# Optimization experiments

Measured on AMD Instinct MI355X. Metric: run time of the kernel, lower is better.

## Reference

```python
import jax, jax.numpy as jnp
import numpy as np

B, T, C = 16, 4096, 1024
MAX_POS, PAD_IDX = 8192, 1


def setup_inputs() -> dict:
    key = jax.random.key(0)
    ks = jax.random.split(key, 6)
    x = jax.random.normal(ks[0], (B, T, C), dtype=jnp.float32)
    lengths = jax.random.randint(ks[1], (B,), 1, T, dtype=jnp.int32)
    padding_mask = jnp.arange(T, dtype=jnp.int32)[None, :] >= lengths[:, None]
    bos_emb = jax.random.normal(ks[2], (C,), dtype=jnp.float32) * 0.02
    eos_emb = jax.random.normal(ks[3], (C,), dtype=jnp.float32) * 0.02
    pos_table = jax.random.normal(ks[4], (MAX_POS + PAD_IDX + 1, C), dtype=jnp.float32) * 0.02
    pos_table = pos_table.at[PAD_IDX].set(0.0)  # padding_idx row is zero in nn.Embedding
    ln_weight = jnp.ones((C,), dtype=jnp.float32)
    ln_bias = jnp.zeros((C,), dtype=jnp.float32)
    return {"x": x, "padding_mask": padding_mask, "lengths": lengths,
            "bos_emb": bos_emb, "eos_emb": eos_emb, "pos_table": pos_table,
            "ln_weight": ln_weight, "ln_bias": ln_bias}


def reference(x, padding_mask, lengths, bos_emb, eos_emb, pos_table, ln_weight, ln_bias):
    b, t, c = x.shape
    # prepend BOS, append a zero slot  -> (B, T+2, C)
    x = jnp.concatenate([
        jnp.broadcast_to(bos_emb, (b, 1, c)).astype(x.dtype),
        x,
        jnp.zeros((b, 1, c), dtype=x.dtype),
    ], axis=1)
    # vectorized per-row EOS scatter: x[i, lengths[i]+1, :] = eos_emb
    x = x.at[jnp.arange(b), lengths + 1].set(eos_emb.astype(x.dtype))
    new_lengths = lengths + 2
    pad_mask = jnp.arange(t + 2, dtype=jnp.int32)[None, :] >= new_lengths[:, None]  # (B, T+2)
    # fairseq make_positions on padding_mask.long() with padding_idx=1:
    # mask = input.ne(padding_idx) -> non-pad; positions = cumsum(mask)*mask + padding_idx
    nonpad = (~pad_mask).astype(jnp.int32)
    positions = jnp.cumsum(nonpad, axis=1) * nonpad + PAD_IDX  # pad slots -> index 1 (zero row)
    pos = pos_table[positions]  # (B, T+2, C)
    y = x + pos
    # LayerNorm over C, eps=1e-5
    mu = jnp.mean(y, axis=-1, keepdims=True)
    var = jnp.mean(jnp.square(y - mu), axis=-1, keepdims=True)
    y = (y - mu) * jax.lax.rsqrt(var + 1e-5) * ln_weight + ln_bias
    return y, pad_mask, new_lengths
```

## Files before the change

kernel.cpp:

```cpp
#include <hip/hip_runtime.h>
#include <hip/hip_bf16.h>

#define B_ 16
#define T_ 4096
#define C_ 1024
#define TP2 (T_ + 2)
#define NROWS (B_ * TP2)

typedef float float4v __attribute__((ext_vector_type(4)));

__global__ __launch_bounds__(256) void embed_ln_kernel(
    const float* __restrict__ x,
    const int*   __restrict__ lengths,
    const float* __restrict__ bos,
    const float* __restrict__ eos,
    const float* __restrict__ pos_table,
    const float* __restrict__ ln_w,
    const float* __restrict__ ln_b,
    float* __restrict__ out_y,
    float* __restrict__ out_mask,
    float* __restrict__ out_len)
{
    const int row  = blockIdx.x * 4 + (threadIdx.x >> 6);
    const int lane = threadIdx.x & 63;
    const int b    = row / TP2;
    const int t    = row - b * TP2;
    const int L    = lengths[b];

    float4v v[4];
    const float4v* srcv = nullptr;
    if (t == 0)          srcv = reinterpret_cast<const float4v*>(bos);
    else if (t == L + 1) srcv = reinterpret_cast<const float4v*>(eos);
    else if (t <= T_)    srcv = reinterpret_cast<const float4v*>(
                                    x + (size_t)(b * T_ + (t - 1)) * C_);
    if (srcv) {
        #pragma unroll
        for (int i = 0; i < 4; ++i)
            v[i] = __builtin_nontemporal_load(&srcv[i * 64 + lane]);
    } else {
        #pragma unroll
        for (int i = 0; i < 4; ++i)
            v[i] = (float4v)(0.f);
    }

    if (t <= L + 1) {
        const float4v* pr = reinterpret_cast<const float4v*>(
                                pos_table + (size_t)(t + 2) * C_);
        #pragma unroll
        for (int i = 0; i < 4; ++i)
            v[i] += pr[i * 64 + lane];
    }

    float s = 0.f, ss = 0.f;
    #pragma unroll
    for (int i = 0; i < 4; ++i) {
        s  += v[i].x + v[i].y + v[i].z + v[i].w;
        ss += v[i].x * v[i].x + v[i].y * v[i].y
            + v[i].z * v[i].z + v[i].w * v[i].w;
    }
    #pragma unroll
    for (int off = 32; off > 0; off >>= 1) {
        s  += __shfl_xor(s,  off);
        ss += __shfl_xor(ss, off);
    }
    const float inv_c = 1.0f / (float)C_;
    const float mu    = s * inv_c;
    const float var   = ss * inv_c - mu * mu;
    const float rstd  = rsqrtf(var + 1e-5f);

    float4v* dst = reinterpret_cast<float4v*>(out_y + (size_t)row * C_);
    const float4v* wv = reinterpret_cast<const float4v*>(ln_w);
    const float4v* bv = reinterpret_cast<const float4v*>(ln_b);
    #pragma unroll
    for (int i = 0; i < 4; ++i) {
        const float4v w  = wv[i * 64 + lane];
        const float4v bb = bv[i * 64 + lane];
        float4v o = (v[i] - mu) * rstd * w + bb;
        __builtin_nontemporal_store(o, &dst[i * 64 + lane]);
    }

    if (lane == 0) {
        out_mask[row] = (t >= L + 2) ? 1.0f : 0.0f;
        if (t == 0) out_len[b] = (float)(L + 2);
    }
}

extern "C" void kernel_launch(void* const* d_in, const int* in_sizes, int n_in,
                              void* d_out, int out_size, void* d_ws, size_t ws_size,
                              hipStream_t stream) {
    const float* x         = (const float*)d_in[0];
    const int*   lengths   = (const int*)d_in[2];
    const float* bos       = (const float*)d_in[3];
    const float* eos       = (const float*)d_in[4];
    const float* pos_table = (const float*)d_in[5];
    const float* ln_w      = (const float*)d_in[6];
    const float* ln_b      = (const float*)d_in[7];

    float* out_y    = (float*)d_out;
    float* out_mask = out_y + (size_t)B_ * TP2 * C_;
    float* out_len  = out_mask + (size_t)B_ * TP2;

    const int grid = NROWS / 4;
    embed_ln_kernel<<<grid, 256, 0, stream>>>(
        x, lengths, bos, eos, pos_table, ln_w, ln_b,
        out_y, out_mask, out_len);
}
```

Before: 102.8 us.

## Process four batches per wave sharing position row and LN params with double-buffered loads

```diff
diff --git a/kernel.cpp b/kernel.cpp
--- a/kernel.cpp
+++ b/kernel.cpp
@@ -5,7 +5,10 @@
 #define T_ 4096
 #define C_ 1024
 #define TP2 (T_ + 2)
-#define NROWS (B_ * TP2)
+#define BPW 4
+#define NGRP (B_ / BPW)
+#define NWAVES (TP2 * NGRP)
+#define NBLK (NWAVES / 4)
 
 typedef float float4v __attribute__((ext_vector_type(4)));
 
@@ -21,68 +24,92 @@
     float* __restrict__ out_mask,
     float* __restrict__ out_len)
 {
-    const int row  = blockIdx.x * 4 + (threadIdx.x >> 6);
+    const int wid  = blockIdx.x * 4 + (threadIdx.x >> 6);
     const int lane = threadIdx.x & 63;
-    const int b    = row / TP2;
-    const int t    = row - b * TP2;
-    const int L    = lengths[b];
+    const int t    = wid >> 2;
+    const int b0   = (wid & 3) * BPW;
 
-    float4v v[4];
-    const float4v* srcv = nullptr;
-    if (t == 0)          srcv = reinterpret_cast<const float4v*>(bos);
-    else if (t == L + 1) srcv = reinterpret_cast<const float4v*>(eos);
-    else if (t <= T_)    srcv = reinterpret_cast<const float4v*>(
-                                    x + (size_t)(b * T_ + (t - 1)) * C_);
-    if (srcv) {
+    float4v w[4], bb[4], ps[4];
+    {
+        const float4v* wv = reinterpret_cast<const float4v*>(ln_w);
+        const float4v* bv = reinterpret_cast<const float4v*>(ln_b);
+        const float4v* pv = reinterpret_cast<const float4v*>(
+                                pos_table + (size_t)(t + 2) * C_);
         #pragma unroll
-        for (int i = 0; i < 4; ++i)
-            v[i] = __builtin_nontemporal_load(&srcv[i * 64 + lane]);
-    } else {
-        #pragma unroll
-        for (int i = 0; i < 4; ++i)
-            v[i] = (float4v)(0.f);
+        for (int i = 0; i < 4; ++i) {
+            w[i]  = wv[i * 64 + lane];
+            bb[i] = bv[i * 64 + lane];
+            ps[i] = pv[i * 64 + lane];
+        }
     }
 
-    if (t <= L + 1) {
-        const float4v* pr = reinterpret_cast<const float4v*>(
-                                pos_table + (size_t)(t + 2) * C_);
+    int L4[BPW];
+    #pragma unroll
+    for (int j = 0; j < BPW; ++j) L4[j] = lengths[b0 + j];
+
+    auto src_of = [&](int j) -> const float4v* {
+        if (t == 0)         return reinterpret_cast<const float4v*>(bos);
+        if (t == L4[j] + 1) return reinterpret_cast<const float4v*>(eos);
+        if (t <= T_)        return reinterpret_cast<const float4v*>(
+                                x + (size_t)((b0 + j) * T_ + (t - 1)) * C_);
+        return nullptr;
+    };
+
+    auto loadrow = [&](float4v (&buf)[4], const float4v* sp) {
+        if (sp) {
+            #pragma unroll
+            for (int i = 0; i < 4; ++i)
+                buf[i] = __builtin_nontemporal_load(&sp[i * 64 + lane]);
+        } else {
+            #pragma unroll
+            for (int i = 0; i < 4; ++i) buf[i] = (float4v)(0.f);
+        }
+    };
+
+    auto process = [&](float4v (&v)[4], int j) {
+        const int L = L4[j];
+        if (t <= L + 1) {
+            #pragma unroll
+            for (int i = 0; i < 4; ++i) v[i] += ps[i];
+        }
+        float s = 0.f, ss = 0.f;
         #pragma unroll
-        for (int i = 0; i < 4; ++i)
-            v[i] += pr[i * 64 + lane];
-    }
+        for (int i = 0; i < 4; ++i) {
+            s  += v[i].x + v[i].y + v[i].z + v[i].w;
+            ss += v[i].x * v[i].x + v[i].y * v[i].y
+                + v[i].z * v[i].z + v[i].w * v[i].w;
+        }
+        #pragma unroll
+        for (int off = 32; off > 0; off >>= 1) {
+            s  += __shfl_xor(s,  off);
+            ss += __shfl_xor(ss, off);
+        }
+        const float inv_c = 1.0f / (float)C_;
+        const float mu   = s * inv_c;
+        const float var  = ss * inv_c - mu * mu;
+        const float rstd = rsqrtf(var + 1e-5f);
+        const int row = (b0 + j) * TP2 + t;
+        float4v* dst = reinterpret_cast<float4v*>(out_y + (size_t)row * C_);
+        #pragma unroll
+        for (int i = 0; i < 4; ++i) {
+            float4v o = (v[i] - mu) * rstd * w[i] + bb[i];
+            __builtin_nontemporal_store(o, &dst[i * 64 + lane]);
+        }
+        if (lane == 0) {
+            out_mask[row] = (t >= L + 2) ? 1.0f : 0.0f;
+            if (t == 0) out_len[b0 + j] = (float)(L + 2);
+        }
+    };
 
-    float s = 0.f, ss = 0.f;
-    #pragma unroll
-    for (int i = 0; i < 4; ++i) {
-        s  += v[i].x + v[i].y + v[i].z + v[i].w;
-        ss += v[i].x * v[i].x + v[i].y * v[i].y
-            + v[i].z * v[i].z + v[i].w * v[i].w;
-    }
-    #pragma unroll
-    for (int off = 32; off > 0; off >>= 1) {
-        s  += __shfl_xor(s,  off);
-        ss += __shfl_xor(ss, off);
-    }
-    const float inv_c = 1.0f / (float)C_;
-    const float mu    = s * inv_c;
-    const float var   = ss * inv_c - mu * mu;
-    const float rstd  = rsqrtf(var + 1e-5f);
-
-    float4v* dst = reinterpret_cast<float4v*>(out_y + (size_t)row * C_);
-    const float4v* wv = reinterpret_cast<const float4v*>(ln_w);
-    const float4v* bv = reinterpret_cast<const float4v*>(ln_b);
-    #pragma unroll
-    for (int i = 0; i < 4; ++i) {
-        const float4v w  = wv[i * 64 + lane];
-        const float4v bb = bv[i * 64 + lane];
-        float4v o = (v[i] - mu) * rstd * w + bb;
-        __builtin_nontemporal_store(o, &dst[i * 64 + lane]);
-    }
-
-    if (lane == 0) {
-        out_mask[row] = (t >= L + 2) ? 1.0f : 0.0f;
-        if (t == 0) out_len[b] = (float)(L + 2);
-    }
+    float4v va[4], vb[4];
+    loadrow(va, src_of(0));
+    loadrow(vb, src_of(1));
+    process(va, 0);
+    loadrow(va, src_of(2));
+    process(vb, 1);
+    loadrow(vb, src_of(3));
+    process(va, 2);
+    process(vb, 3);
 }
 
 extern "C" void kernel_launch(void* const* d_in, const int* in_sizes, int n_in,
@@ -100,8 +127,7 @@
     float* out_mask = out_y + (size_t)B_ * TP2 * C_;
     float* out_len  = out_mask + (size_t)B_ * TP2;
 
-    const int grid = NROWS / 4;
-    embed_ln_kernel<<<grid, 256, 0, stream>>>(
+    embed_ln_kernel<<<NBLK, 256, 0, stream>>>(
         x, lengths, bos, eos, pos_table, ln_w, ln_b,
         out_y, out_mask, out_len);
 }
```

After: 101.7 us. About the same (-1.1%).
